# Kernel tuning notes

Measured on AMD Instinct MI355X. Metric: run time of the kernel, lower is better.

## Reference

```python
import jax, jax.numpy as jnp
import numpy as np

B, S1, S2 = 32, 128, 128
V, D, P, C = 30000, 300, 200, 3


def _highway(x, Wh, bh, Wt, bt):
    h = jax.nn.relu(x @ Wh + bh)
    t = jax.nn.sigmoid(x @ Wt + bt)
    return t * h + (1.0 - t) * x


def _ff(x, W1, b1, W2, b2):
    # self.forward: two relu linear layers (dropout disabled / keep_prob=1)
    return jax.nn.relu(jax.nn.relu(x @ W1 + b1) @ W2 + b2)


def setup_inputs() -> dict:
    key = jax.random.key(0)
    ks = iter(jax.random.split(key, 64))
    W = lambda *s: jax.random.normal(next(ks), s, jnp.float32) * 0.05
    Z = lambda n: jnp.zeros((n,), jnp.float32)
    inp = {
        'x1': jax.random.randint(next(ks), (B, S1), 0, V),
        'x2': jax.random.randint(next(ks), (B, S2), 0, V),
        'emb': jax.random.normal(next(ks), (V, D), jnp.float32),
        'hw1_Wh': W(D, D), 'hw1_bh': Z(D), 'hw1_Wt': W(D, D), 'hw1_bt': Z(D),
        'hw2_Wh': W(D, D), 'hw2_bh': Z(D), 'hw2_Wt': W(D, D), 'hw2_bt': Z(D),
        'mul_W1': W(D, P), 'mul_b1': Z(P), 'mul_W2': W(P, P), 'mul_b2': Z(P),
        'dist_W1': W(D, P), 'dist_b1': Z(P), 'dist_W2': W(P, P), 'dist_b2': Z(P),
        'cmp_W1': W(4 * D, P), 'cmp_b1': Z(P), 'cmp_W2': W(P, P), 'cmp_b2': Z(P),
        'chw1_Wh': W(P, P), 'chw1_bh': Z(P), 'chw1_Wt': W(P, P), 'chw1_bt': Z(P),
        'chw2_Wh': W(P, P), 'chw2_bh': Z(P), 'chw2_Wt': W(P, P), 'chw2_bt': Z(P),
        'agg_W1': W(4 * P, P), 'agg_b1': Z(P), 'agg_W2': W(P, P), 'agg_b2': Z(P),
        'out_W': W(P, C), 'out_b': Z(C),
    }
    return inp


def reference(x1, x2, emb,
              hw1_Wh, hw1_bh, hw1_Wt, hw1_bt,
              hw2_Wh, hw2_bh, hw2_Wt, hw2_bt,
              mul_W1, mul_b1, mul_W2, mul_b2,
              dist_W1, dist_b1, dist_W2, dist_b2,
              cmp_W1, cmp_b1, cmp_W2, cmp_b2,
              chw1_Wh, chw1_bh, chw1_Wt, chw1_bt,
              chw2_Wh, chw2_bh, chw2_Wt, chw2_bt,
              agg_W1, agg_b1, agg_W2, agg_b2,
              out_W, out_b):
    # embed + shared highway stack
    e1 = emb[x1]  # [B,S1,D]
    e2 = emb[x2]  # [B,S2,D]
    e1 = _highway(_highway(e1, hw1_Wh, hw1_bh, hw1_Wt, hw1_bt), hw2_Wh, hw2_bh, hw2_Wt, hw2_bt)
    e2 = _highway(_highway(e2, hw1_Wh, hw1_bh, hw1_Wt, hw1_bt), hw2_Wh, hw2_bh, hw2_Wt, hw2_bt)

    # attention_mul: project both, dot product
    p1 = _ff(e1, mul_W1, mul_b1, mul_W2, mul_b2)  # [B,S1,P]
    p2 = _ff(e2, mul_W1, mul_b1, mul_W2, mul_b2)  # [B,S2,P]
    att1 = jnp.einsum('bip,bjp->bij', p1, p2)

    # attention_dist: project both, sum_d 1/(1+|q1-q2|) -> 4D broadcast
    q1 = _ff(e1, dist_W1, dist_b1, dist_W2, dist_b2)
    q2 = _ff(e2, dist_W1, dist_b1, dist_W2, dist_b2)
    att2 = jnp.sum(1.0 / (1.0 + jnp.abs(q1[:, :, None, :] - q2[:, None, :, :])), axis=-1)

    sim = att1 + att2  # [B,S1,S2]
    alpha = jnp.einsum('bji,bjd->bid', jax.nn.softmax(jnp.swapaxes(sim, 1, 2), axis=-1).transpose(0, 2, 1).transpose(0, 2, 1), e1) if False else jnp.matmul(jax.nn.softmax(jnp.swapaxes(sim, 1, 2), axis=-1), e1)  # [B,S2,D]
    beta = jnp.matmul(jax.nn.softmax(sim, axis=-1), e2)  # [B,S1,D]

    # compare (shared forward + highway stack)
    v1 = _ff(jnp.concatenate([e1, beta, e1 - beta, e1 * beta], -1), cmp_W1, cmp_b1, cmp_W2, cmp_b2)
    v2 = _ff(jnp.concatenate([e2, alpha, e2 - alpha, e2 * alpha], -1), cmp_W1, cmp_b1, cmp_W2, cmp_b2)
    v1 = _highway(_highway(v1, chw1_Wh, chw1_bh, chw1_Wt, chw1_bt), chw2_Wh, chw2_bh, chw2_Wt, chw2_bt)
    v2 = _highway(_highway(v2, chw1_Wh, chw1_bh, chw1_Wt, chw1_bt), chw2_Wh, chw2_bh, chw2_Wt, chw2_bt)

    # aggregate: max + sum pooling, forward, final linear
    v = jnp.concatenate([v1.max(1), v2.max(1), v1.sum(1), v2.sum(1)], -1)  # [B,4P]
    y = _ff(v, agg_W1, agg_b1, agg_W2, agg_b2)
    return y @ out_W + out_b  # [B,C]
```

## Files before the change

kernel.cpp:

```cpp
#include <hip/hip_runtime.h>
#include <hip/hip_bf16.h>
#include <math.h>

#define B_   32
#define S_   128
#define V_   30000
#define D_   300
#define P_   200
#define NT   8192
#define NT1  4096
#define LDE  320
#define LDP  256

typedef __hip_bfloat16 bf16;
typedef __attribute__((ext_vector_type(8))) __bf16 bf16x8;
typedef __attribute__((ext_vector_type(4))) float f32x4;

__device__ __forceinline__ float b2f(bf16 v) { return __bfloat162float(v); }
__device__ __forceinline__ short f2s(float v) { bf16 h = __float2bfloat16(v); return *(short*)&h; }
__device__ __forceinline__ float s2f(short s) { bf16 h; *(short*)&h = s; return __bfloat162float(h); }

struct ConvTable {
    const float* W1[8]; const float* W2[8]; bf16* dst[8];
    int K[8], N1[8], N2[8], Kpad[8], IL[8];
    unsigned long long base[8]; unsigned long long total;
};

__global__ void k_convw(ConvTable T) {
    unsigned long long idx = (unsigned long long)blockIdx.x * 256 + threadIdx.x;
    if (idx >= T.total) return;
    int e = 0;
#pragma unroll
    for (int i = 1; i < 8; ++i) if (idx >= T.base[i]) e = i;
    unsigned long long local = idx - T.base[e];
    int Kpad = T.Kpad[e];
    int n = (int)(local / Kpad);
    int k = (int)(local - (unsigned long long)n * Kpad);
    float v = 0.f;
    if (k < T.K[e]) {
        if (T.IL[e]) {
            int d = n >> 1, half = n & 1;
            if (d < T.N1[e]) v = (half ? T.W2[e] : T.W1[e])[(size_t)k * T.N1[e] + d];
        } else {
            if (n < T.N1[e]) v = T.W1[e][(size_t)k * T.N1[e] + n];
            else if (n < T.N1[e] + T.N2[e]) v = T.W2[e][(size_t)k * T.N2[e] + (n - T.N1[e])];
        }
    }
    T.dst[e][local] = __float2bfloat16(v);
}

__global__ void k_convmisc(const float* __restrict__ Wc, bf16* __restrict__ dstc,
                           const float* __restrict__ A1w, const float* __restrict__ A2w,
                           const float* __restrict__ Ow,
                           float* __restrict__ T1, float* __restrict__ T2,
                           float* __restrict__ T3) {
    int idx = blockIdx.x * 256 + threadIdx.x;
    if (idx < 245760) {
        int n = idx / 960, k = idx - n * 960;
        int sel = k / 320, kc = k - sel * 320;
        float v = 0.f;
        if (kc < 300 && n < 200) {
            if (sel == 0)      v = Wc[(size_t)kc * 200 + n] + Wc[(size_t)(600 + kc) * 200 + n];
            else if (sel == 1) v = Wc[(size_t)(300 + kc) * 200 + n] - Wc[(size_t)(600 + kc) * 200 + n];
            else               v = Wc[(size_t)(900 + kc) * 200 + n];
        }
        dstc[idx] = __float2bfloat16(v);
    } else {
        int l = idx - 245760;
        if (l < 160000)       T1[l] = A1w[(size_t)(l % 800) * 200 + l / 800];
        else if (l < 200000)  { int m = l - 160000; T2[m] = A2w[(size_t)(m % 200) * 200 + m / 200]; }
        else if (l < 200600)  { int m = l - 200000; T3[m] = Ow[(size_t)(m % 200) * 3 + m / 200]; }
    }
}

__global__ void k_embed(const int* __restrict__ x1, const int* __restrict__ x2,
                        const float* __restrict__ emb, bf16* __restrict__ E) {
    int idx = blockIdx.x * 256 + threadIdx.x;
    if (idx >= NT * (LDE / 4)) return;
    int r = idx / (LDE / 4);
    int c4 = (idx - r * (LDE / 4)) * 4;
    int tok = (r < NT1) ? x1[r] : x2[r - NT1];
    if ((unsigned)tok >= (unsigned)V_) tok = 0;
    short o[4];
    if (c4 + 4 <= 300) {
        float4 v = *(const float4*)(emb + (size_t)tok * 300 + c4);
        o[0] = f2s(v.x); o[1] = f2s(v.y); o[2] = f2s(v.z); o[3] = f2s(v.w);
    } else {
#pragma unroll
        for (int i = 0; i < 4; ++i) {
            int c = c4 + i;
            o[i] = f2s((c < 300) ? emb[(size_t)tok * 300 + c] : 0.f);
        }
    }
    *(short4*)((short*)E + (size_t)r * LDE + c4) = *(short4*)&o[0];
}

__global__ __launch_bounds__(256) void k_skinny(
    const float* __restrict__ A, const float* __restrict__ WT,
    const float* __restrict__ bias, float* __restrict__ C,
    int M, int N, int K, int act) {
    int wave = (blockIdx.x * 256 + threadIdx.x) >> 6;
    int lane = threadIdx.x & 63;
    if (wave >= M * N) return;
    int m = wave / N, n = wave - m * N;
    const float4* a4 = (const float4*)(A + (size_t)m * K);
    const float4* w4 = (const float4*)(WT + (size_t)n * K);
    int K4 = K >> 2;
    float acc = 0.f;
    for (int i = lane; i < K4; i += 64) {
        float4 av = a4[i], wv = w4[i];
        acc += av.x * wv.x + av.y * wv.y + av.z * wv.z + av.w * wv.w;
    }
#pragma unroll
    for (int off = 32; off > 0; off >>= 1) acc += __shfl_down(acc, off, 64);
    if (lane == 0) {
        float v = acc + bias[n];
        if (act == 1) v = fmaxf(v, 0.f);
        C[(size_t)m * N + n] = v;
    }
}

template <int AMODE, int EPI>
__global__ __launch_bounds__(256) void k_gemm(
    const bf16* __restrict__ A, const bf16* __restrict__ A2,
    const bf16* __restrict__ A3, int lda,
    const bf16* __restrict__ WT, const bf16* __restrict__ WT2, int Kpad, int K,
    bf16* __restrict__ C, bf16* __restrict__ C2, int ldc, int Ntot, int N1,
    const float* __restrict__ bias1, const float* __restrict__ bias2,
    int act1, int act2, const bf16* __restrict__ xbuf, int ldxb)
{
    __shared__ short As[64][72];
    __shared__ short Bs[64][72];
    int tid = threadIdx.x;
    int w = tid >> 6, lane = tid & 63, quad = lane >> 4, l16 = lane & 15;
    int bm = blockIdx.x * 64;
    int half = 0, bn;
    if (AMODE == 4) { half = blockIdx.y >> 2; bn = (blockIdx.y & 3) * 64; }
    else bn = blockIdx.y * 64;
    const short* Wsh = (const short*)((AMODE == 4 && half) ? WT2 : WT);
    bf16* Cl = (AMODE == 4 && half) ? C2 : C;
    int wr = (w & 1) * 32, wc = (w >> 1) * 32;
    int ar = tid >> 2, ac = (tid & 3) * 16;

    const short* Abase = (const short*)A + (AMODE == 4 ? half * 200 : 0);
    int gm = bm + ar;

    f32x4 acc[2][2];
#pragma unroll
    for (int i = 0; i < 2; ++i)
#pragma unroll
        for (int j = 0; j < 2; ++j)
#pragma unroll
            for (int r = 0; r < 4; ++r) acc[i][j][r] = 0.f;

    short pa[16], pb[16];

    auto loadA = [&](int k0) {
        if (AMODE != 3) {
            int k = k0 + ac;
            const short* src = Abase + (size_t)gm * lda + k;
            if (k + 16 <= K) {
#pragma unroll
                for (int i = 0; i < 4; ++i) *(short4*)&pa[i * 4] = ((const short4*)src)[i];
            } else {
#pragma unroll
                for (int i = 0; i < 16; ++i) pa[i] = (k + i < K) ? src[i] : (short)0;
            }
        } else {
            int sel = k0 / 320;
            const short* base = (sel == 0) ? (const short*)A
                              : (sel == 1) ? (const short*)A2 : (const short*)A3;
            int k = (k0 - sel * 320) + ac;
            const short* src = base + (size_t)gm * LDE + k;
            if (k + 16 <= 300) {
#pragma unroll
                for (int i = 0; i < 4; ++i) *(short4*)&pa[i * 4] = ((const short4*)src)[i];
            } else {
#pragma unroll
                for (int i = 0; i < 16; ++i) pa[i] = (k + i < 300) ? src[i] : (short)0;
            }
        }
    };
    auto loadB = [&](int k0) {
        const short* src = Wsh + (size_t)(bn + ar) * Kpad + k0 + ac;
#pragma unroll
        for (int i = 0; i < 4; ++i) *(short4*)&pb[i * 4] = ((const short4*)src)[i];
    };

    loadA(0); loadB(0);
    for (int k0 = 0; k0 < Kpad; k0 += 64) {
#pragma unroll
        for (int i = 0; i < 4; ++i) {
            *(short4*)&As[ar][ac + i * 4] = *(short4*)&pa[i * 4];
            *(short4*)&Bs[ar][ac + i * 4] = *(short4*)&pb[i * 4];
        }
        __syncthreads();
        if (k0 + 64 < Kpad) { loadA(k0 + 64); loadB(k0 + 64); }
        {
            bf16x8 a[2][2], b[2][2];
#pragma unroll
            for (int mt = 0; mt < 2; ++mt)
#pragma unroll
                for (int ks = 0; ks < 2; ++ks)
                    a[mt][ks] = *(const bf16x8*)&As[wr + mt * 16 + l16][ks * 32 + quad * 8];
#pragma unroll
            for (int nt = 0; nt < 2; ++nt)
#pragma unroll
                for (int ks = 0; ks < 2; ++ks)
                    b[nt][ks] = *(const bf16x8*)&Bs[wc + nt * 16 + l16][ks * 32 + quad * 8];
#pragma unroll
            for (int mt = 0; mt < 2; ++mt)
#pragma unroll
                for (int nt = 0; nt < 2; ++nt) {
                    acc[mt][nt] = __builtin_amdgcn_mfma_f32_16x16x32_bf16(a[mt][0], b[nt][0], acc[mt][nt], 0, 0, 0);
                    acc[mt][nt] = __builtin_amdgcn_mfma_f32_16x16x32_bf16(a[mt][1], b[nt][1], acc[mt][nt], 0, 0, 0);
                }
        }
        __syncthreads();
    }
    short (*Cs)[72] = As;
#pragma unroll
    for (int mt = 0; mt < 2; ++mt) {
#pragma unroll
        for (int nt = 0; nt < 2; ++nt) {
            int cl = wc + nt * 16 + l16;
            int col = bn + cl;
            float bv; int act;
            if (EPI == 1) {
                int d = col >> 1;
                if (d > N1 - 1) d = N1 - 1;
                if (col & 1) { bv = bias2[d]; act = 2; }
                else         { bv = bias1[d]; act = 1; }
            } else if (AMODE == 4) {
                int cc = (col < N1) ? col : (N1 - 1);
                bv = (half ? bias2 : bias1)[cc]; act = act1;
            } else {
                int cc = (col < Ntot) ? col : (Ntot - 1);
                if (cc < N1) { bv = bias1[cc]; act = act1; }
                else { bv = bias2[cc - N1]; act = act2; }
            }
#pragma unroll
            for (int r = 0; r < 4; ++r) {
                float v = acc[mt][nt][r] + bv;
                if (act == 1) v = fmaxf(v, 0.f);
                else if (act == 2) v = 1.f / (1.f + expf(-v));
                Cs[wr + mt * 16 + quad * 4 + r][cl] = f2s(v);
            }
        }
    }
    __syncthreads();
    if (EPI == 0) {
#pragma unroll
        for (int it = 0; it < 2; ++it) {
            int chunk = tid + it * 256;
            int rl = chunk >> 3;
            int c8 = (chunk & 7) * 8;
            short* dst = (short*)Cl + (size_t)(bm + rl) * ldc + bn + c8;
            *(short4*)dst = *(short4*)&Cs[rl][c8];
            *(short4*)(dst + 4) = *(short4*)&Cs[rl][c8 + 4];
        }
    } else {
        int d0 = bn >> 1;
#pragma unroll
        for (int it = 0; it < 2; ++it) {
            int chunk = tid + it * 256;
            int rl = chunk >> 3;
            int c4 = (chunk & 7) * 4;
            int row = bm + rl;
            const short* xs = (const short*)xbuf + (size_t)row * ldxb + d0 + c4;
            short o[4];
#pragma unroll
            for (int i = 0; i < 4; ++i) {
                float h = s2f(Cs[rl][2 * (c4 + i)]);
                float t = s2f(Cs[rl][2 * (c4 + i) + 1]);
                o[i] = f2s(t * h + (1.f - t) * s2f(xs[i]));
            }
            *(short4*)((short*)Cl + (size_t)row * ldc + d0 + c4) = *(short4*)&o[0];
        }
    }
}

__global__ void k_transpose2(const bf16* __restrict__ srcP, bf16* __restrict__ dstP,
                             const bf16* __restrict__ srcQ, bf16* __restrict__ dstQ) {
    int idx = blockIdx.x * 256 + threadIdx.x;
    if (idx >= B_ * P_ * S_) return;
    const bf16* src = blockIdx.y ? srcQ : srcP;
    bf16* dst = blockIdx.y ? dstQ : dstP;
    int j = idx & (S_ - 1);
    int rest = idx >> 7;
    int p = rest % P_;
    int b = rest / P_;
    dst[idx] = src[((size_t)(b * S_ + j)) * LDP + p];
}

__global__ __launch_bounds__(256) void k_sim2(const bf16* __restrict__ Pmat,
                                              const bf16* __restrict__ Qmat,
                                              const bf16* __restrict__ PT,
                                              const bf16* __restrict__ QT,
                                              float* __restrict__ SIM) {
    __shared__ float qp[8][P_][2];
    int blk = blockIdx.x;
    int b = blk >> 4;
    int it = blk & 15;
    int tid = threadIdx.x;
    int j = tid & 127, h = tid >> 7;
    int row0 = b * 128 + it * 8;
    for (int x = tid; x < 8 * P_; x += 256) {
        int r = x / P_, c = x - r * P_;
        qp[r][c][0] = b2f(Qmat[(size_t)(row0 + r) * LDP + c]);
        qp[r][c][1] = b2f(Pmat[(size_t)(row0 + r) * LDP + c]);
    }
    __syncthreads();
    const bf16* ptb = PT + (size_t)b * P_ * S_;
    const bf16* qtb = QT + (size_t)b * P_ * S_;
    float acc[4] = {0.f, 0.f, 0.f, 0.f};
    for (int p = 0; p < P_; ++p) {
        float v = b2f(ptb[p * S_ + j]);
        float u = b2f(qtb[p * S_ + j]);
#pragma unroll
        for (int r = 0; r < 4; ++r) {
            int i = h * 4 + r;
            float2 w = *(const float2*)&qp[i][p][0];
            float d = w.x - u;
            acc[r] += w.y * v + __builtin_amdgcn_rcpf(1.f + fabsf(d));
        }
    }
#pragma unroll
    for (int r = 0; r < 4; ++r) {
        int i = it * 8 + h * 4 + r;
        SIM[((size_t)(b * 128 + i)) * S_ + j] = acc[r];
    }
}

__global__ __launch_bounds__(256) void k_av2(const float* __restrict__ SIM,
                                             const bf16* __restrict__ E,
                                             bf16* __restrict__ OUT,
                                             bf16* __restrict__ EA) {
    int blk = blockIdx.x;
    int kind = blk >> 12;
    int blk2 = blk & 4095;
    int b = blk2 >> 7, r = blk2 & 127;
    int t = threadIdx.x;
    __shared__ float w[S_];
    __shared__ float red[S_];
    float x = 0.f;
    if (t < 128) {
        x = (kind == 0) ? SIM[(size_t)blk2 * S_ + t]
                        : SIM[((size_t)b * S_ + t) * S_ + r];
        red[t] = x;
    }
    __syncthreads();
    for (int s = 64; s > 0; s >>= 1) {
        if (t < s) red[t] = fmaxf(red[t], red[t + s]);
        __syncthreads();
    }
    float mx = red[0];
    __syncthreads();
    float ex = 0.f;
    if (t < 128) { ex = expf(x - mx); red[t] = ex; }
    __syncthreads();
    for (int s = 64; s > 0; s >>= 1) {
        if (t < s) red[t] += red[t + s];
        __syncthreads();
    }
    if (t < 128) w[t] = ex / red[0];
    __syncthreads();
    if (t < 150) {
        int orow_idx = (kind == 0) ? blk2 : (NT1 + blk2);
        const bf16* Esrc = E + (kind == 0 ? (size_t)NT1 * LDE : 0) + (size_t)b * S_ * LDE;
        const unsigned short* ebase = (const unsigned short*)Esrc + 2 * t;
        float a0 = 0.f, a1 = 0.f;
        for (int s = 0; s < S_; ++s) {
            unsigned int uv = *(const unsigned int*)(ebase + (size_t)s * LDE);
            float lo = __uint_as_float(uv << 16);
            float hi = __uint_as_float(uv & 0xffff0000u);
            float ws = w[s];
            a0 += ws * lo;
            a1 += ws * hi;
        }
        unsigned int o = (unsigned int)(unsigned short)f2s(a0)
                       | ((unsigned int)(unsigned short)f2s(a1) << 16);
        *(unsigned int*)((unsigned short*)OUT + (size_t)orow_idx * LDE + 2 * t) = o;
        unsigned int ev = *(const unsigned int*)((const unsigned short*)E + (size_t)orow_idx * LDE + 2 * t);
        float e0 = __uint_as_float(ev << 16);
        float e1 = __uint_as_float(ev & 0xffff0000u);
        unsigned int o2 = (unsigned int)(unsigned short)f2s(a0 * e0)
                        | ((unsigned int)(unsigned short)f2s(a1 * e1) << 16);
        *(unsigned int*)((unsigned short*)EA + (size_t)orow_idx * LDE + 2 * t) = o2;
    }
}

__global__ __launch_bounds__(256) void k_pool(const bf16* __restrict__ V,
                                              float* __restrict__ OUT) {
    int b = blockIdx.x;
    int c = threadIdx.x;
    if (c >= P_) return;
    const bf16* v1 = V + (size_t)(b * S_) * LDP;
    const bf16* v2 = V + (size_t)(NT1 + b * S_) * LDP;
    float mx1 = -INFINITY, mx2 = -INFINITY, s1 = 0.f, s2 = 0.f;
    for (int i = 0; i < S_; ++i) {
        float a = b2f(v1[(size_t)i * LDP + c]);
        mx1 = fmaxf(mx1, a); s1 += a;
        float bb = b2f(v2[(size_t)i * LDP + c]);
        mx2 = fmaxf(mx2, bb); s2 += bb;
    }
    float* o = OUT + (size_t)b * 4 * P_;
    o[c] = mx1; o[P_ + c] = mx2; o[2 * P_ + c] = s1; o[3 * P_ + c] = s2;
}

__global__ void k_fillf(float* dst, int n, float v) {
    int i = blockIdx.x * 256 + threadIdx.x;
    if (i < n) dst[i] = v;
}

extern "C" void kernel_launch(void* const* d_in, const int* in_sizes, int n_in,
                              void* d_out, int out_size, void* d_ws, size_t ws_size,
                              hipStream_t stream) {
    const int* x1 = (const int*)d_in[0];
    const int* x2 = (const int*)d_in[1];
    const float* emb = (const float*)d_in[2];
    const float *hw1_Wh = (const float*)d_in[3],  *hw1_bh = (const float*)d_in[4];
    const float *hw1_Wt = (const float*)d_in[5],  *hw1_bt = (const float*)d_in[6];
    const float *hw2_Wh = (const float*)d_in[7],  *hw2_bh = (const float*)d_in[8];
    const float *hw2_Wt = (const float*)d_in[9],  *hw2_bt = (const float*)d_in[10];
    const float *mul_W1 = (const float*)d_in[11], *mul_b1 = (const float*)d_in[12];
    const float *mul_W2 = (const float*)d_in[13], *mul_b2 = (const float*)d_in[14];
    const float *dist_W1 = (const float*)d_in[15], *dist_b1 = (const float*)d_in[16];
    const float *dist_W2 = (const float*)d_in[17], *dist_b2 = (const float*)d_in[18];
    const float *cmp_W1 = (const float*)d_in[19], *cmp_b1 = (const float*)d_in[20];
    const float *cmp_W2 = (const float*)d_in[21], *cmp_b2 = (const float*)d_in[22];
    const float *chw1_Wh = (const float*)d_in[23], *chw1_bh = (const float*)d_in[24];
    const float *chw1_Wt = (const float*)d_in[25], *chw1_bt = (const float*)d_in[26];
    const float *chw2_Wh = (const float*)d_in[27], *chw2_bh = (const float*)d_in[28];
    const float *chw2_Wt = (const float*)d_in[29], *chw2_bt = (const float*)d_in[30];
    const float *agg_W1 = (const float*)d_in[31], *agg_b1 = (const float*)d_in[32];
    const float *agg_W2 = (const float*)d_in[33], *agg_b2 = (const float*)d_in[34];
    const float *out_W = (const float*)d_in[35], *out_b = (const float*)d_in[36];

    const size_t nE = (size_t)NT * LDE;
    const size_t nP = (size_t)NT * LDP;
    const size_t nCht = (size_t)NT * 448;
    const size_t nTR = (size_t)B_ * P_ * S_;
    const size_t nWT = 1224704;
    size_t bf16_elems = 4 * nE + 2 * nP + 2 * nCht + nWT;
    size_t f32_elems = (size_t)B_ * 4 * P_ + 2 * (size_t)B_ * P_ + 200600;
    size_t need = bf16_elems * 2 + f32_elems * 4 + 64;
    if (ws_size < need) {
        k_fillf<<<dim3(1), dim3(256), 0, stream>>>((float*)d_out, B_ * 3, 555.f);
        return;
    }
    bf16* Eb  = (bf16*)d_ws;
    bf16* X1  = Eb + nE;
    bf16* X2  = X1 + nE;
    bf16* EA  = X2 + nE;
    bf16* Pb  = EA + nE;
    bf16* Qb  = Pb + nP;
    bf16* ChtA = Qb + nP;
    bf16* ChtB = ChtA + nCht;
    bf16* WTp = ChtB + nCht;
    float* POOL = (float*)(WTp + nWT);
    float* G1 = POOL + (size_t)B_ * 4 * P_;
    float* G2 = G1 + (size_t)B_ * P_;
    float* WT_a1 = G2 + (size_t)B_ * P_;
    float* WT_a2 = WT_a1 + 160000;
    float* WT_o  = WT_a2 + 40000;
    bf16* ATT = Eb;
    bf16* PTb = ChtB;
    bf16* QTb = ChtB + nTR;
    float* SIM = (float*)(ChtB + 2 * nTR);
    bf16* V2 = ChtB;

    bf16* WT_hw1 = WTp + 0;
    bf16* WT_hw2 = WTp + 204800;
    bf16* WT_md  = WTp + 409600;
    bf16* WT_m2  = WTp + 552960;
    bf16* WT_d2  = WTp + 618496;
    bf16* WT_c2  = WTp + 684032;
    bf16* WT_ch1 = WTp + 749568;
    bf16* WT_ch2 = WTp + 864256;
    bf16* WT_c1  = WTp + 978944;

    dim3 blk256(256);

    ConvTable T;
    const float* s1[8] = {hw1_Wh, hw2_Wh, mul_W1, mul_W2, dist_W2, cmp_W2, chw1_Wh, chw2_Wh};
    const float* s2[8] = {hw1_Wt, hw2_Wt, dist_W1, nullptr, nullptr, nullptr, chw1_Wt, chw2_Wt};
    bf16* dsts[8] = {WT_hw1, WT_hw2, WT_md, WT_m2, WT_d2, WT_c2, WT_ch1, WT_ch2};
    int Ks[8]  = {300, 300, 300, 200, 200, 200, 200, 200};
    int N1s[8] = {300, 300, 200, 200, 200, 200, 200, 200};
    int N2s[8] = {300, 300, 200, 0, 0, 0, 200, 200};
    int Kps[8] = {320, 320, 320, 256, 256, 256, 256, 256};
    int Nps[8] = {640, 640, 448, 256, 256, 256, 448, 448};
    int ILs[8] = {1, 1, 0, 0, 0, 0, 1, 1};
    unsigned long long base = 0;
    for (int i = 0; i < 8; ++i) {
        T.W1[i] = s1[i]; T.W2[i] = s2[i]; T.dst[i] = dsts[i];
        T.K[i] = Ks[i]; T.N1[i] = N1s[i]; T.N2[i] = N2s[i]; T.Kpad[i] = Kps[i];
        T.IL[i] = ILs[i];
        T.base[i] = base;
        base += (unsigned long long)Kps[i] * Nps[i];
    }
    T.total = base;
    k_convw<<<dim3((unsigned)((base + 255) / 256)), blk256, 0, stream>>>(T);
    k_convmisc<<<dim3((245760 + 200600 + 255) / 256), blk256, 0, stream>>>(
        cmp_W1, WT_c1, agg_W1, agg_W2, out_W, WT_a1, WT_a2, WT_o);

    k_embed<<<dim3((NT * (LDE / 4) + 255) / 256), blk256, 0, stream>>>(x1, x2, emb, Eb);

    k_gemm<0, 1><<<dim3(128, 10), blk256, 0, stream>>>(
        Eb, nullptr, nullptr, LDE,
        WT_hw1, nullptr, 320, 300, X1, nullptr, LDE, 600, 300,
        hw1_bh, hw1_bt, 1, 2, Eb, LDE);

    k_gemm<0, 1><<<dim3(128, 10), blk256, 0, stream>>>(
        X1, nullptr, nullptr, LDE,
        WT_hw2, nullptr, 320, 300, X2, nullptr, LDE, 600, 300,
        hw2_bh, hw2_bt, 1, 2, X1, LDE);

    k_gemm<0, 0><<<dim3(128, 7), blk256, 0, stream>>>(
        X2, nullptr, nullptr, LDE,
        WT_md, nullptr, 320, 300, ChtA, nullptr, 448, 400, 200,
        mul_b1, dist_b1, 1, 1, nullptr, 0);

    k_gemm<4, 0><<<dim3(128, 8), blk256, 0, stream>>>(
        ChtA, nullptr, nullptr, 448,
        WT_m2, WT_d2, 256, 200, Pb, Qb, LDP, 256, 200,
        mul_b2, dist_b2, 1, 1, nullptr, 0);

    int nTRb = (int)((nTR + 255) / 256);
    k_transpose2<<<dim3(nTRb, 2), blk256, 0, stream>>>(
        Pb + (size_t)NT1 * LDP, PTb, Qb + (size_t)NT1 * LDP, QTb);

    k_sim2<<<dim3(B_ * 16), blk256, 0, stream>>>(Pb, Qb, PTb, QTb, SIM);

    k_av2<<<dim3(2 * NT1), blk256, 0, stream>>>(SIM, X2, ATT, EA);

    k_gemm<3, 0><<<dim3(128, 4), blk256, 0, stream>>>(
        X2, ATT, EA, LDE,
        WT_c1, nullptr, 960, 300, ChtA, nullptr, LDP, 200, 200,
        cmp_b1, cmp_b1, 1, 1, nullptr, 0);

    k_gemm<0, 0><<<dim3(128, 4), blk256, 0, stream>>>(
        ChtA, nullptr, nullptr, LDP,
        WT_c2, nullptr, 256, 200, Pb, nullptr, LDP, 200, 200,
        cmp_b2, cmp_b2, 1, 1, nullptr, 0);

    k_gemm<0, 1><<<dim3(128, 7), blk256, 0, stream>>>(
        Pb, nullptr, nullptr, LDP,
        WT_ch1, nullptr, 256, 200, Qb, nullptr, LDP, 400, 200,
        chw1_bh, chw1_bt, 1, 2, Pb, LDP);

    k_gemm<0, 1><<<dim3(128, 7), blk256, 0, stream>>>(
        Qb, nullptr, nullptr, LDP,
        WT_ch2, nullptr, 256, 200, V2, nullptr, LDP, 400, 200,
        chw2_bh, chw2_bt, 1, 2, Qb, LDP);

    k_pool<<<dim3(B_), blk256, 0, stream>>>(V2, POOL);

    k_skinny<<<dim3(1600), blk256, 0, stream>>>(POOL, WT_a1, agg_b1, G1, B_, P_, 800, 1);
    k_skinny<<<dim3(1600), blk256, 0, stream>>>(G1, WT_a2, agg_b2, G2, B_, P_, 200, 1);
    k_skinny<<<dim3(24), blk256, 0, stream>>>(G2, WT_o, out_b, (float*)d_out, B_, 3, 200, 0);
}
```

Measured before the change: 337.2 us.

## Split softmax from attention matmul and run weighted sum on MFMA

The fused softmax-plus-weighted-sum kernel is split in two. A softmax kernel writes normalized bf16 attention weights to a scratch buffer, and a tiled MFMA GEMM kernel computes the attention-weighted embeddings and the elementwise product output. This replaces the per-row scalar FMA loop, which reread each batch's embedding block once per row, with shared-memory-tiled bf16 matrix-core work. The cost is an extra launch, a round trip of the weight matrix through global memory, and weights rounded to bf16. The grid covers 320 columns, so padded columns past 300 are also computed and written.

```diff
diff --git a/kernel.cpp b/kernel.cpp
--- a/kernel.cpp
+++ b/kernel.cpp
@@ -332,23 +332,17 @@
     }
 }
 
-__global__ __launch_bounds__(256) void k_av2(const float* __restrict__ SIM,
-                                             const bf16* __restrict__ E,
-                                             bf16* __restrict__ OUT,
-                                             bf16* __restrict__ EA) {
+__global__ __launch_bounds__(128) void k_soft(const float* __restrict__ SIM,
+                                              bf16* __restrict__ Wb) {
     int blk = blockIdx.x;
     int kind = blk >> 12;
     int blk2 = blk & 4095;
     int b = blk2 >> 7, r = blk2 & 127;
     int t = threadIdx.x;
-    __shared__ float w[S_];
-    __shared__ float red[S_];
-    float x = 0.f;
-    if (t < 128) {
-        x = (kind == 0) ? SIM[(size_t)blk2 * S_ + t]
-                        : SIM[((size_t)b * S_ + t) * S_ + r];
-        red[t] = x;
-    }
+    __shared__ float red[128];
+    float x = (kind == 0) ? SIM[(size_t)blk2 * S_ + t]
+                          : SIM[((size_t)(b * S_ + t)) * S_ + r];
+    red[t] = x;
     __syncthreads();
     for (int s = 64; s > 0; s >>= 1) {
         if (t < s) red[t] = fmaxf(red[t], red[t + s]);
@@ -356,37 +350,118 @@
     }
     float mx = red[0];
     __syncthreads();
-    float ex = 0.f;
-    if (t < 128) { ex = expf(x - mx); red[t] = ex; }
+    float ex = expf(x - mx);
+    red[t] = ex;
     __syncthreads();
     for (int s = 64; s > 0; s >>= 1) {
         if (t < s) red[t] += red[t + s];
         __syncthreads();
     }
-    if (t < 128) w[t] = ex / red[0];
+    Wb[(size_t)blk * 128 + t] = __float2bfloat16(ex / red[0]);
+}
+
+__global__ __launch_bounds__(256) void k_attg(const bf16* __restrict__ Wb,
+                                              const bf16* __restrict__ E,
+                                              bf16* __restrict__ ATT,
+                                              bf16* __restrict__ EA) {
+    __shared__ short As[64][72];
+    __shared__ short Bs[64][72];
+    int tid = threadIdx.x;
+    int w = tid >> 6, lane = tid & 63, quad = lane >> 4, l16 = lane & 15;
+    int m0 = blockIdx.x * 64;
+    int kind = (m0 >= NT1) ? 1 : 0;
+    int local = m0 - kind * NT1;
+    int b = local >> 7;
+    int ebase = kind ? (b * 128) : (NT1 + b * 128);
+    int bn = blockIdx.y * 64;
+    int wr = (w & 1) * 32, wc = (w >> 1) * 32;
+    int ar = tid >> 2, ac = (tid & 3) * 16;
+
+    f32x4 acc[2][2];
+#pragma unroll
+    for (int i = 0; i < 2; ++i)
+#pragma unroll
+        for (int j = 0; j < 2; ++j)
+#pragma unroll
+            for (int r = 0; r < 4; ++r) acc[i][j][r] = 0.f;
+
+    for (int k0 = 0; k0 < 128; k0 += 64) {
+        {
+            const short* src = (const short*)Wb + (size_t)(m0 + ar) * 128 + k0 + ac;
+#pragma unroll
+            for (int i = 0; i < 4; ++i) *(short4*)&As[ar][ac + i * 4] = ((const short4*)src)[i];
+        }
+#pragma unroll
+        for (int it = 0; it < 2; ++it) {
+            int idx = tid + it * 256;
+            int r = idx >> 3;
+            int c8 = (idx & 7) * 8;
+            const short* src = (const short*)E + (size_t)(ebase + k0 + r) * LDE + bn + c8;
+            short4 v0 = ((const short4*)src)[0];
+            short4 v1 = ((const short4*)src)[1];
+            const short* vp = (const short*)&v0;
+#pragma unroll
+            for (int i = 0; i < 4; ++i) Bs[c8 + i][r] = vp[i];
+            vp = (const short*)&v1;
+#pragma unroll
+            for (int i = 0; i < 4; ++i) Bs[c8 + 4 + i][r] = vp[i];
+        }
+        __syncthreads();
+        {
+            bf16x8 a[2][2], bb[2][2];
+#pragma unroll
+            for (int mt = 0; mt < 2; ++mt)
+#pragma unroll
+                for (int ks = 0; ks < 2; ++ks)
+                    a[mt][ks] = *(const bf16x8*)&As[wr + mt * 16 + l16][ks * 32 + quad * 8];
+#pragma unroll
+            for (int nt = 0; nt < 2; ++nt)
+#pragma unroll
+                for (int ks = 0; ks < 2; ++ks)
+                    bb[nt][ks] = *(const bf16x8*)&Bs[wc + nt * 16 + l16][ks * 32 + quad * 8];
+#pragma unroll
+            for (int mt = 0; mt < 2; ++mt)
+#pragma unroll
+                for (int nt = 0; nt < 2; ++nt) {
+                    acc[mt][nt] = __builtin_amdgcn_mfma_f32_16x16x32_bf16(a[mt][0], bb[nt][0], acc[mt][nt], 0, 0, 0);
+                    acc[mt][nt] = __builtin_amdgcn_mfma_f32_16x16x32_bf16(a[mt][1], bb[nt][1], acc[mt][nt], 0, 0, 0);
+                }
+        }
+        __syncthreads();
+    }
+    short (*Cs)[72] = As;
+#pragma unroll
+    for (int mt = 0; mt < 2; ++mt)
+#pragma unroll
+        for (int nt = 0; nt < 2; ++nt) {
+            int cl = wc + nt * 16 + l16;
+#pragma unroll
+            for (int r = 0; r < 4; ++r)
+                Cs[wr + mt * 16 + quad * 4 + r][cl] = f2s(acc[mt][nt][r]);
+        }
     __syncthreads();
-    if (t < 150) {
-        int orow_idx = (kind == 0) ? blk2 : (NT1 + blk2);
-        const bf16* Esrc = E + (kind == 0 ? (size_t)NT1 * LDE : 0) + (size_t)b * S_ * LDE;
-        const unsigned short* ebase = (const unsigned short*)Esrc + 2 * t;
-        float a0 = 0.f, a1 = 0.f;
-        for (int s = 0; s < S_; ++s) {
-            unsigned int uv = *(const unsigned int*)(ebase + (size_t)s * LDE);
-            float lo = __uint_as_float(uv << 16);
-            float hi = __uint_as_float(uv & 0xffff0000u);
-            float ws = w[s];
-            a0 += ws * lo;
-            a1 += ws * hi;
-        }
-        unsigned int o = (unsigned int)(unsigned short)f2s(a0)
-                       | ((unsigned int)(unsigned short)f2s(a1) << 16);
-        *(unsigned int*)((unsigned short*)OUT + (size_t)orow_idx * LDE + 2 * t) = o;
-        unsigned int ev = *(const unsigned int*)((const unsigned short*)E + (size_t)orow_idx * LDE + 2 * t);
-        float e0 = __uint_as_float(ev << 16);
-        float e1 = __uint_as_float(ev & 0xffff0000u);
-        unsigned int o2 = (unsigned int)(unsigned short)f2s(a0 * e0)
-                        | ((unsigned int)(unsigned short)f2s(a1 * e1) << 16);
-        *(unsigned int*)((unsigned short*)EA + (size_t)orow_idx * LDE + 2 * t) = o2;
+#pragma unroll
+    for (int it = 0; it < 2; ++it) {
+        int chunk = tid + it * 256;
+        int rl = chunk >> 3;
+        int c8 = (chunk & 7) * 8;
+        int row = m0 + rl;
+        short a8[8];
+        *(short4*)&a8[0] = *(short4*)&Cs[rl][c8];
+        *(short4*)&a8[4] = *(short4*)&Cs[rl][c8 + 4];
+        short* adst = (short*)ATT + (size_t)row * LDE + bn + c8;
+        *(short4*)adst = *(short4*)&a8[0];
+        *(short4*)(adst + 4) = *(short4*)&a8[4];
+        const short* es = (const short*)E + (size_t)row * LDE + bn + c8;
+        short e8[8];
+        *(short4*)&e8[0] = ((const short4*)es)[0];
+        *(short4*)&e8[4] = ((const short4*)es)[1];
+        short o8[8];
+#pragma unroll
+        for (int i = 0; i < 8; ++i) o8[i] = f2s(s2f(a8[i]) * s2f(e8[i]));
+        short* edst = (short*)EA + (size_t)row * LDE + bn + c8;
+        *(short4*)edst = *(short4*)&o8[0];
+        *(short4*)(edst + 4) = *(short4*)&o8[4];
     }
 }
 
@@ -465,6 +540,7 @@
     float* WT_a2 = WT_a1 + 160000;
     float* WT_o  = WT_a2 + 40000;
     bf16* ATT = Eb;
+    bf16* Wbuf = ChtA;
     bf16* PTb = ChtB;
     bf16* QTb = ChtB + nTR;
     float* SIM = (float*)(ChtB + 2 * nTR);
@@ -533,7 +609,9 @@
 
     k_sim2<<<dim3(B_ * 16), blk256, 0, stream>>>(Pb, Qb, PTb, QTb, SIM);
 
-    k_av2<<<dim3(2 * NT1), blk256, 0, stream>>>(SIM, X2, ATT, EA);
+    k_soft<<<dim3(2 * NT1), dim3(128), 0, stream>>>(SIM, Wbuf);
+
+    k_attg<<<dim3(128, 5), blk256, 0, stream>>>(Wbuf, X2, ATT, EA);
 
     k_gemm<3, 0><<<dim3(128, 4), blk256, 0, stream>>>(
         X2, ATT, EA, LDE,
```

Result: faster. 318.3 us (-5.6%).
